# Kernel optimization log

Hardware: AMD Instinct MI355X
Metric: run time of the kernel (lower is better)

## Reference

```python
import jax, jax.numpy as jnp
import numpy as np

BS, S, E, H = 64, 512, 1024, 16
HD = E // H
MASK_ID, KNOW_ID = 30001, 30002


def setup_inputs() -> dict:
    key = jax.random.key(0)
    ks = jax.random.split(key, 8)
    model_output = jax.random.normal(ks[0], (BS, S, E), dtype=jnp.float32)
    ids = jax.random.randint(ks[1], (BS, S), 0, 30000)  # never hits special ids
    ids = ids.at[:, 0].set(MASK_ID)        # exactly one [MASK] per sequence
    ids = ids.at[:, 1:9].set(KNOW_ID)      # 8 knowledge slots per sequence
    knowledge_output = jax.random.normal(ks[2], (BS, E), dtype=jnp.float32)
    empty_knowledge_mask = jax.random.randint(ks[3], (BS,), 0, 2).astype(bool)
    bound = 1.0 / np.sqrt(E)
    in_proj_weight = jax.random.uniform(ks[4], (3 * E, E), minval=-bound, maxval=bound, dtype=jnp.float32)
    in_proj_bias = jnp.zeros((3 * E,), jnp.float32)
    out_proj_weight = jax.random.uniform(ks[5], (E, E), minval=-bound, maxval=bound, dtype=jnp.float32)
    out_proj_bias = jnp.zeros((E,), jnp.float32)
    attention_strength = jnp.float32(0.1)
    return {
        "model_output": model_output,
        "knowledge_output": knowledge_output,
        "in_proj_weight": in_proj_weight,
        "in_proj_bias": in_proj_bias,
        "out_proj_weight": out_proj_weight,
        "out_proj_bias": out_proj_bias,
        "attention_strength": attention_strength,
        "input_ids": ids,
        "empty_knowledge_mask": empty_knowledge_mask,
        "knowledge_token_id": KNOW_ID,
        "mask_token_id": MASK_ID,
    }


def reference(model_output, knowledge_output, in_proj_weight, in_proj_bias,
              out_proj_weight, out_proj_bias, attention_strength,
              input_ids, empty_knowledge_mask, knowledge_token_id, mask_token_id):
    bs, sent_len, hidden = model_output.shape
    # --- knowledge injection: scatter knowledge vector into knowledge-token slots ---
    knowledge_mask = input_ids == knowledge_token_id                 # [bs, S]
    kv_src = jnp.where(knowledge_mask[:, :, None],
                       knowledge_output[:, None, :], model_output)  # [bs, S, E]
    # --- single-query gather: one [MASK] position per sequence ---
    mask_pos = jnp.argmax(input_ids == mask_token_id, axis=1)        # [bs]
    q_in = jnp.take_along_axis(kv_src, mask_pos[:, None, None], axis=1)[:, 0, :]  # [bs, E]
    # --- nn.MultiheadAttention (eval mode, dropout=0) ---
    Wq, Wk, Wv = in_proj_weight[:E], in_proj_weight[E:2 * E], in_proj_weight[2 * E:]
    bq, bk, bv = in_proj_bias[:E], in_proj_bias[E:2 * E], in_proj_bias[2 * E:]
    q = (q_in @ Wq.T + bq).reshape(bs, H, HD)                        # [bs, H, hd]
    k = (kv_src @ Wk.T + bk).reshape(bs, sent_len, H, HD)            # [bs, S, H, hd]
    v = (kv_src @ Wv.T + bv).reshape(bs, sent_len, H, HD)
    scale = 1.0 / np.sqrt(HD)
    scores = jnp.einsum('bhd,bshd->bhs', q * scale, k)               # [bs, H, S]
    attn = jax.nn.softmax(scores, axis=-1)
    ctx = jnp.einsum('bhs,bshd->bhd', attn, v).reshape(bs, hidden)   # [bs, E]
    attn_output = ctx @ out_proj_weight.T + out_proj_bias            # [bs, E]
    # --- residual on the ORIGINAL (pre-injection) mask-token states ---
    origin_q = jnp.take_along_axis(model_output, mask_pos[:, None, None], axis=1)[:, 0, :]
    mask_output = origin_q + attention_strength * attn_output
    # --- conditional restore where knowledge is empty ---
    mask_output = jnp.where(empty_knowledge_mask[:, None], origin_q, mask_output)
    return mask_output
```

## Files before the change

### kernel.cpp

```cpp
#include <hip/hip_runtime.h>

#define BS 64
#define S  512
#define E  1024
#define H  16
#define HD 64
#define SCALE 0.125f
#define CATT 8

#define W_QIN  1024
#define W_QKBF 66560
#define W_NUM  1115136
#define W_DEN  9503744
#define W_CTX  9511936

typedef __attribute__((ext_vector_type(8))) short short8;
typedef __attribute__((ext_vector_type(4))) float floatx4;

union S8u { uint2 u2[2]; short8 s; };

__device__ __forceinline__ unsigned short bf16c(float x) {
    unsigned int u = __float_as_uint(x);
    return (unsigned short)((u + 0x7fffu + ((u >> 16) & 1u)) >> 16);
}
__device__ __forceinline__ unsigned int pack_bf16(float a, float b) {
    return (unsigned int)bf16c(a) | ((unsigned int)bf16c(b) << 16);
}
__device__ __forceinline__ void fma4(float4& acc, float s, const float4& v) {
    acc.x += s * v.x; acc.y += s * v.y; acc.z += s * v.z; acc.w += s * v.w;
}
__device__ __forceinline__ float dot4(const float4& a, const float4& b) {
    return a.x * b.x + a.y * b.y + a.z * b.z + a.w * b.w;
}
__device__ __forceinline__ void bfly8(float* a) {
    #pragma unroll
    for (int off = 32; off > 0; off >>= 1) {
        #pragma unroll
        for (int i = 0; i < 8; i++) a[i] += __shfl_xor(a[i], off, 64);
    }
}

__global__ void k_prep(const float* __restrict__ model, const float* __restrict__ knowledge,
                       const int* __restrict__ ids, const int* __restrict__ mask_id_p,
                       const int* __restrict__ kid_p, int* __restrict__ mp,
                       float* __restrict__ qin) {
    int b = blockIdx.x, tid = threadIdx.x;
    __shared__ int best;
    if (tid == 0) best = S;
    __syncthreads();
    int mid = mask_id_p[0];
    for (int s = tid; s < S; s += 256)
        if (ids[b * S + s] == mid) atomicMin(&best, s);
    __syncthreads();
    int m = (best == S) ? 0 : best;
    if (tid == 0) mp[b] = m;
    bool isk = (ids[b * S + m] == kid_p[0]);
    const float* qrow = isk ? knowledge + (size_t)b * E : model + ((size_t)(b * S + m)) * E;
    ((float4*)(qin + (size_t)b * E))[tid] = ((const float4*)qrow)[tid];
}

__global__ void k_qgen(const float* __restrict__ qin, const float* __restrict__ w_in,
                       const float* __restrict__ b_in, unsigned short* __restrict__ qkbf) {
    int h = blockIdx.x, b0 = blockIdx.y * 4, t = threadIdx.x;
    __shared__ float qin_l[4][1024];
    __shared__ float qred[4][64][4];
    __shared__ float qs_l[4][64];
    #pragma unroll
    for (int k = 0; k < 4; k++) {
        int idx4 = k * 256 + t;
        int bb = idx4 >> 8, col = (idx4 & 255) * 4;
        *(float4*)&qin_l[bb][col] = *(const float4*)(qin + (size_t)(b0 + bb) * E + col);
    }
    __syncthreads();
    {
        int d = t >> 2, part = t & 3;
        const float* wr = w_in + (size_t)(h * HD + d) * E + part * 256;
        float acc[4] = {0.f, 0.f, 0.f, 0.f};
        #pragma unroll 8
        for (int i = 0; i < 64; i++) {
            float4 wv = *(const float4*)(wr + i * 4);
            #pragma unroll
            for (int bb = 0; bb < 4; bb++)
                acc[bb] += dot4(wv, *(const float4*)&qin_l[bb][part * 256 + i * 4]);
        }
        #pragma unroll
        for (int bb = 0; bb < 4; bb++) qred[bb][d][part] = acc[bb];
    }
    __syncthreads();
    if (t < 64) {
        float bias = b_in[h * HD + t];
        #pragma unroll
        for (int bb = 0; bb < 4; bb++)
            qs_l[bb][t] = qred[bb][t][0] + qred[bb][t][1] + qred[bb][t][2] + qred[bb][t][3] + bias;
    }
    __syncthreads();
    {
        int e0 = t * 4;
        const float* wk = w_in + (size_t)(E + h * HD) * E + e0;
        float4 acc[4];
        #pragma unroll
        for (int bb = 0; bb < 4; bb++) acc[bb] = make_float4(0.f, 0.f, 0.f, 0.f);
        #pragma unroll 8
        for (int d = 0; d < HD; d++) {
            float4 wv = *(const float4*)(wk + (size_t)d * E);
            #pragma unroll
            for (int bb = 0; bb < 4; bb++) fma4(acc[bb], qs_l[bb][d], wv);
        }
        #pragma unroll
        for (int bb = 0; bb < 4; bb++) {
            uint2 pk;
            pk.x = pack_bf16(acc[bb].x * SCALE, acc[bb].y * SCALE);
            pk.y = pack_bf16(acc[bb].z * SCALE, acc[bb].w * SCALE);
            *(uint2*)&qkbf[((size_t)(b0 + bb) * H + h) * E + e0] = pk;
        }
    }
}

__global__ __launch_bounds__(512, 4) void k_attn(
    const float* __restrict__ model, const float* __restrict__ knowledge,
    const int* __restrict__ ids, const int* __restrict__ kid_p,
    const unsigned short* __restrict__ qkbf, unsigned short* __restrict__ num,
    float* __restrict__ den) {
    __shared__ __align__(16) unsigned char Ubuf[73984];
    unsigned short* Rbuf  = (unsigned short*)Ubuf;
    unsigned short* RbufT = (unsigned short*)(Ubuf + 33024);
    unsigned short* TbufH = (unsigned short*)Ubuf;
    __shared__ unsigned short Pbuf[16 * 40];
    __shared__ float Sred[4][16][17];
    __shared__ unsigned long long kmask_s;

    int tid = threadIdx.x;
    int w = tid >> 6, l = tid & 63;
    int quad = l >> 4, lm = l & 15;
    int c = blockIdx.x, b = blockIdx.y;
    int s0 = c * 64;

    if (w == 0) {
        int id = ids[b * S + s0 + l];
        unsigned long long mk = __ballot(id == kid_p[0]);
        if (l == 0) kmask_s = mk;
    }
    floatx4 accn[8];
    #pragma unroll
    for (int i = 0; i < 8; i++) accn[i] = (floatx4)0.f;
    float accden = 0.f;
    const float* kb = knowledge + (size_t)b * E;
    const float* mb = model + (size_t)b * S * E;
    const unsigned short* qh = qkbf + ((size_t)b * H + lm) * E;
    __syncthreads();
    unsigned long long kmask = kmask_s;

    for (int pass = 0; pass < 4; pass++) {
        int rb = pass * 16;
        #pragma unroll
        for (int g = 0; g < 4; g++) {
            int r0 = g * 4;
            const float* rp0 = ((kmask >> (rb + r0 + 0)) & 1ull) ? kb : mb + (size_t)(s0 + rb + r0 + 0) * E;
            const float* rp1 = ((kmask >> (rb + r0 + 1)) & 1ull) ? kb : mb + (size_t)(s0 + rb + r0 + 1) * E;
            const float* rp2 = ((kmask >> (rb + r0 + 2)) & 1ull) ? kb : mb + (size_t)(s0 + rb + r0 + 2) * E;
            const float* rp3 = ((kmask >> (rb + r0 + 3)) & 1ull) ? kb : mb + (size_t)(s0 + rb + r0 + 3) * E;
            #pragma unroll
            for (int cc = 0; cc < 2; cc++) {
                int col = cc * 512 + tid;
                unsigned short h0 = bf16c(rp0[col]);
                unsigned short h1 = bf16c(rp1[col]);
                unsigned short h2 = bf16c(rp2[col]);
                unsigned short h3 = bf16c(rp3[col]);
                Rbuf[(r0 + 0) * 1032 + col] = h0;
                Rbuf[(r0 + 1) * 1032 + col] = h1;
                Rbuf[(r0 + 2) * 1032 + col] = h2;
                Rbuf[(r0 + 3) * 1032 + col] = h3;
                uint2 pk;
                pk.x = (unsigned int)h0 | ((unsigned int)h1 << 16);
                pk.y = (unsigned int)h2 | ((unsigned int)h3 << 16);
                *(uint2*)&RbufT[col * 20 + r0] = pk;
            }
        }
        __syncthreads();
        if (w < 4) {
            floatx4 acs = (floatx4)0.f;
            #pragma unroll
            for (int t = 0; t < 8; t++) {
                int kk = w * 8 + t;
                short8 a  = *(const short8*)(const void*)&Rbuf[lm * 1032 + kk * 32 + quad * 8];
                short8 bf = *(const short8*)(const void*)(qh + kk * 32 + quad * 8);
                acs = __builtin_amdgcn_mfma_f32_16x16x32_bf16(a, bf, acs, 0, 0, 0);
            }
            Sred[w][quad * 4 + 0][lm] = acs[0];
            Sred[w][quad * 4 + 1][lm] = acs[1];
            Sred[w][quad * 4 + 2][lm] = acs[2];
            Sred[w][quad * 4 + 3][lm] = acs[3];
        }
        __syncthreads();
        if (w == 0) {
            float ex[4];
            #pragma unroll
            for (int r = 0; r < 4; r++) {
                int row = quad * 4 + r;
                float s = Sred[0][row][lm] + Sred[1][row][lm] + Sred[2][row][lm] + Sred[3][row][lm];
                ex[r] = __expf(s);
                accden += ex[r];
            }
            uint2 pw;
            pw.x = (unsigned int)bf16c(ex[0]) | ((unsigned int)bf16c(ex[1]) << 16);
            pw.y = (unsigned int)bf16c(ex[2]) | ((unsigned int)bf16c(ex[3]) << 16);
            *(uint2*)&Pbuf[lm * 40 + quad * 4] = pw;
        }
        __syncthreads();
        short8 afr = {};
        if (quad < 2) afr = *(const short8*)(const void*)&Pbuf[lm * 40 + quad * 8];
        #pragma unroll
        for (int i = 0; i < 8; i++) {
            int e = (w * 8 + i) * 16 + lm;
            S8u bb; bb.s = (short8){};
            if (quad < 2) {
                bb.u2[0] = *(const uint2*)&RbufT[e * 20 + quad * 8];
                bb.u2[1] = *(const uint2*)&RbufT[e * 20 + quad * 8 + 4];
            }
            accn[i] = __builtin_amdgcn_mfma_f32_16x16x32_bf16(afr, bb.s, accn[i], 0, 0, 0);
        }
        __syncthreads();
    }
    #pragma unroll
    for (int i = 0; i < 8; i++) {
        int e = (w * 8 + i) * 16 + lm;
        TbufH[(quad * 4 + 0) * 1024 + e] = bf16c(accn[i][0]);
        TbufH[(quad * 4 + 1) * 1024 + e] = bf16c(accn[i][1]);
        TbufH[(quad * 4 + 2) * 1024 + e] = bf16c(accn[i][2]);
        TbufH[(quad * 4 + 3) * 1024 + e] = bf16c(accn[i][3]);
    }
    if (w == 0) {
        accden += __shfl_xor(accden, 16, 64);
        accden += __shfl_xor(accden, 32, 64);
        if (l < 16) den[(size_t)(c * BS + b) * H + l] = accden;
    }
    __syncthreads();
    uint4* numv = (uint4*)(num + ((size_t)(c * BS + b) * H) * E);
    const uint4* tb = (const uint4*)TbufH;
    #pragma unroll
    for (int k = 0; k < 4; k++)
        numv[k * 512 + tid] = tb[k * 512 + tid];
}

__global__ void k_pc(const unsigned short* __restrict__ num, const float* __restrict__ den,
                     const float* __restrict__ w_in, const float* __restrict__ b_in,
                     float* __restrict__ ctx) {
    int h = blockIdx.x, b0 = blockIdx.y * 4, t = threadIdx.x;
    __shared__ float p_l[4][1024];
    __shared__ float cred[4][64][4];
    __shared__ float inv_l[4];
    #pragma unroll
    for (int k = 0; k < 4; k++) {
        int idx4 = k * 256 + t;
        int bb = idx4 >> 8, e4 = (idx4 & 255) * 4;
        float4 a = make_float4(0.f, 0.f, 0.f, 0.f);
        #pragma unroll
        for (int cc = 0; cc < CATT; cc++) {
            uint2 v = *(const uint2*)(num + (((size_t)(cc * BS + b0 + bb) * H + h) * E) + e4);
            a.x += __uint_as_float(v.x << 16);
            a.y += __uint_as_float(v.x & 0xffff0000u);
            a.z += __uint_as_float(v.y << 16);
            a.w += __uint_as_float(v.y & 0xffff0000u);
        }
        *(float4*)&p_l[bb][e4] = a;
    }
    if (t < 4) {
        float ds = 0.f;
        for (int cc = 0; cc < CATT; cc++) ds += den[(size_t)(cc * BS + b0 + t) * H + h];
        inv_l[t] = 1.0f / ds;
    }
    __syncthreads();
    {
        int jj = t >> 2, part = t & 3;
        const float* wr = w_in + (size_t)(2 * E + h * HD + jj) * E + part * 256;
        float acc[4] = {0.f, 0.f, 0.f, 0.f};
        #pragma unroll 8
        for (int i = 0; i < 64; i++) {
            float4 wv = *(const float4*)(wr + i * 4);
            #pragma unroll
            for (int bb = 0; bb < 4; bb++)
                acc[bb] += dot4(wv, *(const float4*)&p_l[bb][part * 256 + i * 4]);
        }
        #pragma unroll
        for (int bb = 0; bb < 4; bb++) cred[bb][jj][part] = acc[bb];
    }
    __syncthreads();
    if (t < 64) {
        float bias = b_in[2 * E + h * HD + t];
        #pragma unroll
        for (int bb = 0; bb < 4; bb++) {
            float s = cred[bb][t][0] + cred[bb][t][1] + cred[bb][t][2] + cred[bb][t][3];
            ctx[(size_t)(b0 + bb) * E + h * HD + t] = inv_l[bb] * s + bias;
        }
    }
}

__global__ void k_out(const float* __restrict__ model, const float* __restrict__ w_out,
                      const float* __restrict__ b_out, const float* __restrict__ ctx,
                      const int* __restrict__ mp, const int* __restrict__ empty,
                      const float* __restrict__ strength_p, float* __restrict__ out) {
    int w = threadIdx.x >> 6, l = threadIdx.x & 63;
    int j = blockIdx.x * 4 + w;
    int b0 = blockIdx.y * 8;
    const float* wr = w_out + (size_t)j * E;
    float4 wv[4];
    #pragma unroll
    for (int r = 0; r < 4; r++) wv[r] = *(const float4*)(wr + r * 256 + l * 4);
    float acc[8];
    #pragma unroll
    for (int bb = 0; bb < 8; bb++) {
        const float* src = ctx + (size_t)(b0 + bb) * E;
        float a = 0.f;
        #pragma unroll
        for (int r = 0; r < 4; r++) a += dot4(wv[r], *(const float4*)(src + r * 256 + l * 4));
        acc[bb] = a;
    }
    bfly8(acc);
    if (l < 8) {
        float myacc = acc[0];
        #pragma unroll
        for (int bb = 1; bb < 8; bb++) myacc = (l == bb) ? acc[bb] : myacc;
        int b = b0 + l;
        int m = mp[b];
        float orig = model[((size_t)(b * S + m)) * E + j];
        float bias = b_out[j];
        float st = strength_p[0];
        out[(size_t)b * E + j] = empty[b] ? orig : orig + st * (myacc + bias);
    }
}

extern "C" void kernel_launch(void* const* d_in, const int* in_sizes, int n_in,
                              void* d_out, int out_size, void* d_ws, size_t ws_size,
                              hipStream_t stream) {
    const float* model     = (const float*)d_in[0];
    const float* knowledge = (const float*)d_in[1];
    const float* w_in      = (const float*)d_in[2];
    const float* b_in      = (const float*)d_in[3];
    const float* w_out     = (const float*)d_in[4];
    const float* b_out     = (const float*)d_in[5];
    const float* strength  = (const float*)d_in[6];
    const int*   ids       = (const int*)d_in[7];
    const int*   empty     = (const int*)d_in[8];
    const int*   know_id   = (const int*)d_in[9];
    const int*   mask_id   = (const int*)d_in[10];
    float* out = (float*)d_out;

    float* ws  = (float*)d_ws;
    int*   mp  = (int*)d_ws;
    float* qin = ws + W_QIN;
    unsigned short* qkbf = (unsigned short*)(ws + W_QKBF);
    unsigned short* num  = (unsigned short*)(ws + W_NUM);
    float* den = ws + W_DEN;
    float* ctx = ws + W_CTX;

    k_prep<<<BS, 256, 0, stream>>>(model, knowledge, ids, mask_id, know_id, mp, qin);
    k_qgen<<<dim3(H, 16), 256, 0, stream>>>(qin, w_in, b_in, qkbf);
    k_attn<<<dim3(CATT, BS), 512, 0, stream>>>(model, knowledge, ids, know_id, qkbf, num, den);
    k_pc<<<dim3(H, 16), 256, 0, stream>>>(num, den, w_in, b_in, ctx);
    k_out<<<dim3(256, 8), 256, 0, stream>>>(model, w_out, b_out, ctx, mp, empty, strength, out);
}
```

Measured before the change: 279.5 us.

## Prefetch next row tile into registers, spread softmax across waves, widen num loads

```diff
diff --git a/kernel.cpp b/kernel.cpp
--- a/kernel.cpp
+++ b/kernel.cpp
@@ -127,6 +127,7 @@
     unsigned short* TbufH = (unsigned short*)Ubuf;
     __shared__ unsigned short Pbuf[16 * 40];
     __shared__ float Sred[4][16][17];
+    __shared__ float denp[4][16];
     __shared__ unsigned long long kmask_s;
 
     int tid = threadIdx.x;
@@ -150,33 +151,61 @@
     __syncthreads();
     unsigned long long kmask = kmask_s;
 
+    int rgA = tid >> 8;
+    int c4  = tid & 255;
+
+    float4 st[8];
+
+    auto ISSUE = [&](int pass) {
+        int rb = pass * 16;
+        #pragma unroll
+        for (int j = 0; j < 4; j++) {
+            int row = rb + rgA * 4 + j;
+            const float* rp = ((kmask >> row) & 1ull) ? kb : mb + (size_t)(s0 + row) * E;
+            st[j] = *(const float4*)(rp + c4 * 4);
+        }
+        #pragma unroll
+        for (int j = 0; j < 4; j++) {
+            int row = rb + (rgA + 2) * 4 + j;
+            const float* rp = ((kmask >> row) & 1ull) ? kb : mb + (size_t)(s0 + row) * E;
+            st[4 + j] = *(const float4*)(rp + c4 * 4);
+        }
+    };
+    auto STORE = [&]() {
+        #pragma unroll
+        for (int u = 0; u < 2; u++) {
+            int rg = rgA + u * 2;
+            unsigned short hh[4][4];
+            #pragma unroll
+            for (int j = 0; j < 4; j++) {
+                float4 v = st[u * 4 + j];
+                hh[j][0] = bf16c(v.x); hh[j][1] = bf16c(v.y);
+                hh[j][2] = bf16c(v.z); hh[j][3] = bf16c(v.w);
+            }
+            #pragma unroll
+            for (int j = 0; j < 4; j++) {
+                uint2 pk;
+                pk.x = (unsigned int)hh[j][0] | ((unsigned int)hh[j][1] << 16);
+                pk.y = (unsigned int)hh[j][2] | ((unsigned int)hh[j][3] << 16);
+                *(uint2*)&Rbuf[(rg * 4 + j) * 1032 + c4 * 4] = pk;
+            }
+            #pragma unroll
+            for (int k = 0; k < 4; k++) {
+                uint2 pk;
+                pk.x = (unsigned int)hh[0][k] | ((unsigned int)hh[1][k] << 16);
+                pk.y = (unsigned int)hh[2][k] | ((unsigned int)hh[3][k] << 16);
+                *(uint2*)&RbufT[(c4 * 4 + k) * 20 + rg * 4] = pk;
+            }
+        }
+    };
+
+    ISSUE(0);
+    STORE();
+    __syncthreads();
+
+    #pragma unroll
     for (int pass = 0; pass < 4; pass++) {
-        int rb = pass * 16;
-        #pragma unroll
-        for (int g = 0; g < 4; g++) {
-            int r0 = g * 4;
-            const float* rp0 = ((kmask >> (rb + r0 + 0)) & 1ull) ? kb : mb + (size_t)(s0 + rb + r0 + 0) * E;
-            const float* rp1 = ((kmask >> (rb + r0 + 1)) & 1ull) ? kb : mb + (size_t)(s0 + rb + r0 + 1) * E;
-            const float* rp2 = ((kmask >> (rb + r0 + 2)) & 1ull) ? kb : mb + (size_t)(s0 + rb + r0 + 2) * E;
-            const float* rp3 = ((kmask >> (rb + r0 + 3)) & 1ull) ? kb : mb + (size_t)(s0 + rb + r0 + 3) * E;
-            #pragma unroll
-            for (int cc = 0; cc < 2; cc++) {
-                int col = cc * 512 + tid;
-                unsigned short h0 = bf16c(rp0[col]);
-                unsigned short h1 = bf16c(rp1[col]);
-                unsigned short h2 = bf16c(rp2[col]);
-                unsigned short h3 = bf16c(rp3[col]);
-                Rbuf[(r0 + 0) * 1032 + col] = h0;
-                Rbuf[(r0 + 1) * 1032 + col] = h1;
-                Rbuf[(r0 + 2) * 1032 + col] = h2;
-                Rbuf[(r0 + 3) * 1032 + col] = h3;
-                uint2 pk;
-                pk.x = (unsigned int)h0 | ((unsigned int)h1 << 16);
-                pk.y = (unsigned int)h2 | ((unsigned int)h3 << 16);
-                *(uint2*)&RbufT[col * 20 + r0] = pk;
-            }
-        }
-        __syncthreads();
+        if (pass < 3) ISSUE(pass + 1);
         if (w < 4) {
             floatx4 acs = (floatx4)0.f;
             #pragma unroll
@@ -192,34 +221,33 @@
             Sred[w][quad * 4 + 3][lm] = acs[3];
         }
         __syncthreads();
-        if (w == 0) {
-            float ex[4];
-            #pragma unroll
-            for (int r = 0; r < 4; r++) {
-                int row = quad * 4 + r;
-                float s = Sred[0][row][lm] + Sred[1][row][lm] + Sred[2][row][lm] + Sred[3][row][lm];
-                ex[r] = __expf(s);
-                accden += ex[r];
-            }
-            uint2 pw;
-            pw.x = (unsigned int)bf16c(ex[0]) | ((unsigned int)bf16c(ex[1]) << 16);
-            pw.y = (unsigned int)bf16c(ex[2]) | ((unsigned int)bf16c(ex[3]) << 16);
-            *(uint2*)&Pbuf[lm * 40 + quad * 4] = pw;
+        if (w < 4) {
+            int row = w * 4 + quad;
+            float s = Sred[0][row][lm] + Sred[1][row][lm] + Sred[2][row][lm] + Sred[3][row][lm];
+            float ex = __expf(s);
+            accden += ex;
+            Pbuf[lm * 40 + row] = bf16c(ex);
         }
         __syncthreads();
-        short8 afr = {};
-        if (quad < 2) afr = *(const short8*)(const void*)&Pbuf[lm * 40 + quad * 8];
-        #pragma unroll
-        for (int i = 0; i < 8; i++) {
-            int e = (w * 8 + i) * 16 + lm;
-            S8u bb; bb.s = (short8){};
-            if (quad < 2) {
-                bb.u2[0] = *(const uint2*)&RbufT[e * 20 + quad * 8];
-                bb.u2[1] = *(const uint2*)&RbufT[e * 20 + quad * 8 + 4];
-            }
-            accn[i] = __builtin_amdgcn_mfma_f32_16x16x32_bf16(afr, bb.s, accn[i], 0, 0, 0);
+        {
+            short8 afr = {};
+            if (quad < 2) afr = *(const short8*)(const void*)&Pbuf[lm * 40 + quad * 8];
+            #pragma unroll
+            for (int i = 0; i < 8; i++) {
+                int e = (w * 8 + i) * 16 + lm;
+                S8u bb2; bb2.s = (short8){};
+                if (quad < 2) {
+                    bb2.u2[0] = *(const uint2*)&RbufT[e * 20 + quad * 8];
+                    bb2.u2[1] = *(const uint2*)&RbufT[e * 20 + quad * 8 + 4];
+                }
+                accn[i] = __builtin_amdgcn_mfma_f32_16x16x32_bf16(afr, bb2.s, accn[i], 0, 0, 0);
+            }
         }
         __syncthreads();
+        if (pass < 3) {
+            STORE();
+            __syncthreads();
+        }
     }
     #pragma unroll
     for (int i = 0; i < 8; i++) {
@@ -229,12 +257,14 @@
         TbufH[(quad * 4 + 2) * 1024 + e] = bf16c(accn[i][2]);
         TbufH[(quad * 4 + 3) * 1024 + e] = bf16c(accn[i][3]);
     }
-    if (w == 0) {
+    if (w < 4) {
         accden += __shfl_xor(accden, 16, 64);
         accden += __shfl_xor(accden, 32, 64);
-        if (l < 16) den[(size_t)(c * BS + b) * H + l] = accden;
-    }
-    __syncthreads();
+        if (l < 16) denp[w][l] = accden;
+    }
+    __syncthreads();
+    if (w == 0 && l < 16)
+        den[(size_t)(c * BS + b) * H + l] = denp[0][l] + denp[1][l] + denp[2][l] + denp[3][l];
     uint4* numv = (uint4*)(num + ((size_t)(c * BS + b) * H) * E);
     const uint4* tb = (const uint4*)TbufH;
     #pragma unroll
@@ -250,19 +280,24 @@
     __shared__ float cred[4][64][4];
     __shared__ float inv_l[4];
     #pragma unroll
-    for (int k = 0; k < 4; k++) {
-        int idx4 = k * 256 + t;
-        int bb = idx4 >> 8, e4 = (idx4 & 255) * 4;
-        float4 a = make_float4(0.f, 0.f, 0.f, 0.f);
+    for (int k = 0; k < 2; k++) {
+        int idx8 = k * 256 + t;
+        int bb = idx8 >> 7, e8 = (idx8 & 127) * 8;
+        float a0 = 0.f, a1 = 0.f, a2 = 0.f, a3 = 0.f, a4 = 0.f, a5 = 0.f, a6 = 0.f, a7 = 0.f;
         #pragma unroll
         for (int cc = 0; cc < CATT; cc++) {
-            uint2 v = *(const uint2*)(num + (((size_t)(cc * BS + b0 + bb) * H + h) * E) + e4);
-            a.x += __uint_as_float(v.x << 16);
-            a.y += __uint_as_float(v.x & 0xffff0000u);
-            a.z += __uint_as_float(v.y << 16);
-            a.w += __uint_as_float(v.y & 0xffff0000u);
-        }
-        *(float4*)&p_l[bb][e4] = a;
+            uint4 v = *(const uint4*)(num + (((size_t)(cc * BS + b0 + bb) * H + h) * E) + e8);
+            a0 += __uint_as_float(v.x << 16);
+            a1 += __uint_as_float(v.x & 0xffff0000u);
+            a2 += __uint_as_float(v.y << 16);
+            a3 += __uint_as_float(v.y & 0xffff0000u);
+            a4 += __uint_as_float(v.z << 16);
+            a5 += __uint_as_float(v.z & 0xffff0000u);
+            a6 += __uint_as_float(v.w << 16);
+            a7 += __uint_as_float(v.w & 0xffff0000u);
+        }
+        *(float4*)&p_l[bb][e8]     = make_float4(a0, a1, a2, a3);
+        *(float4*)&p_l[bb][e8 + 4] = make_float4(a4, a5, a6, a7);
     }
     if (t < 4) {
         float ds = 0.f;
```

Result: no change. 281.4 us (+0.7%).
